# Kernel tuning notes

Hardware: AMD Instinct MI355X
Metric: run time of the kernel (lower is better)

Reference implementation:

```python
import jax, jax.numpy as jnp
import numpy as np

N = 100000        # nodes
E = 1600000       # edges
F_IN = 128        # input features
H = 64            # hidden
B = 256           # graphs in batch
MIN_SCORE = 1e-3  # SAGPooling min_score
TOL = 1e-7        # PyG topk tolerance
NEG = jnp.float32(-1e30)


def setup_inputs() -> dict:
    key = jax.random.key(0)
    ks = jax.random.split(key, 24)
    x = jax.random.normal(ks[0], (N, F_IN), jnp.float32)
    src = jax.random.randint(ks[1], (E,), 0, N, dtype=jnp.int32)
    dst = jax.random.randint(ks[2], (E,), 0, N, dtype=jnp.int32)
    batch = jnp.sort(jax.random.randint(ks[3], (N,), 0, B, dtype=jnp.int32))
    node_attention = jax.random.uniform(ks[4], (N,), jnp.float32)

    def lin(k, i, o):
        return jax.random.normal(k, (i, o), jnp.float32) / np.float32(np.sqrt(i))

    p = {
        'W11': lin(ks[5], F_IN, H), 'b11': jnp.zeros((H,), jnp.float32),
        'W12': lin(ks[6], H, H),    'b12': jnp.zeros((H,), jnp.float32),
        'gW1': lin(ks[7], H, 1),    'gb1': jnp.zeros((1,), jnp.float32),
        'W21': lin(ks[8], H, H),    'b21': jnp.zeros((H,), jnp.float32),
        'W22': lin(ks[9], H, H),    'b22': jnp.zeros((H,), jnp.float32),
        'gW2': lin(ks[10], H, 1),   'gb2': jnp.zeros((1,), jnp.float32),
        'W31': lin(ks[11], H, H),   'b31': jnp.zeros((H,), jnp.float32),
        'W32': lin(ks[12], H, H),   'b32': jnp.zeros((H,), jnp.float32),
        'Wl':  lin(ks[13], H, 1),   'bl': jnp.zeros((1,), jnp.float32),
    }
    return dict(x=x, src=src, dst=dst, batch=batch, node_attention=node_attention, **p)


def gin_conv(x, src, dst, emask, W1, b1, W2, b2):
    # GINConv, eps=0: mlp(x + sum_{j in N(i)} x_j), edges masked by emask
    agg = jax.ops.segment_sum(x[src] * emask[:, None], dst, num_segments=N)
    h = x + agg
    return jax.nn.relu(h @ W1 + b1) @ W2 + b2


def gcn_attn(x, src, dst, emask, nmask, W, b):
    # GCNConv(H,1) with self-loops + symmetric normalization on the masked graph
    h = x @ W  # [N,1]
    deg = jax.ops.segment_sum(emask, dst, num_segments=N) + nmask
    dinv = jnp.where(deg > 0, jax.lax.rsqrt(jnp.maximum(deg, 1e-12)), 0.0)
    coef = dinv[src] * dinv[dst] * emask
    out = jax.ops.segment_sum(h[src] * coef[:, None], dst, num_segments=N)
    out = out + h * (dinv * dinv * nmask)[:, None] + b
    return out[:, 0]


def seg_softmax(a, batch, nmask):
    am = jnp.where(nmask > 0, a, NEG)
    m = jax.ops.segment_max(am, batch, num_segments=B)
    e = jnp.where(nmask > 0, jnp.exp(a - m[batch]), 0.0)
    s = jax.ops.segment_sum(e, batch, num_segments=B)
    return e / jnp.maximum(s[batch], 1e-30)


def sag_pool(x, src, dst, emask, nmask, batch, W, b):
    attn = gcn_attn(x, src, dst, emask, nmask, W, b)
    score = seg_softmax(attn, batch, nmask)
    smax = jax.ops.segment_max(jnp.where(nmask > 0, score, NEG), batch, num_segments=B)
    thr = jnp.minimum(MIN_SCORE, smax[batch] - TOL)
    keep = ((nmask > 0) & (score > thr)).astype(x.dtype)
    x2 = x * (score * keep)[:, None]          # x[perm] * score[perm], masked form
    emask2 = emask * keep[src] * keep[dst]    # filter_adj
    return x2, emask2, keep, score


def reference(x, src, dst, batch, node_attention,
              W11, b11, W12, b12, gW1, gb1,
              W21, b21, W22, b22, gW2, gb2,
              W31, b31, W32, b32, Wl, bl):
    emask = jnp.ones((E,), x.dtype)
    nmask0 = jnp.ones((N,), x.dtype)

    h = jax.nn.relu(gin_conv(x, src, dst, emask, W11, b11, W12, b12))
    h, emask, keep1, _ = sag_pool(h, src, dst, emask, nmask0, batch, gW1, gb1)

    h = jax.nn.relu(gin_conv(h, src, dst, emask, W21, b21, W22, b22))
    h, emask, keep2, score2 = sag_pool(h, src, dst, emask, keep1, batch, gW2, gb2)

    ratio = jnp.sum(keep2) / jnp.float32(N)

    h = jax.nn.relu(gin_conv(h, src, dst, emask, W31, b31, W32, b32))

    # global max pool over surviving nodes
    hm = jnp.where(keep2[:, None] > 0, h, NEG)
    g = jax.ops.segment_max(hm, batch, num_segments=B)
    out = g @ Wl + bl  # [B,1]

    # attention KL loss; perm2 indexes the pool1-compacted array (as in the source)
    r1 = jnp.clip(jnp.cumsum(keep1).astype(jnp.int32) - 1, 0, N - 1)
    t = node_attention[r1]
    logp = jnp.log(score2 + 1e-14)
    kl = jnp.where(t > 0, t * jnp.log(jnp.maximum(t, 1e-38)), 0.0) - t * logp
    kl = kl * keep2
    s = jax.ops.segment_sum(kl, batch, num_segments=B)
    c = jax.ops.segment_sum(keep2, batch, num_segments=B)
    attn_loss = s / jnp.maximum(c, 1.0)  # scatter_mean

    return out, attn_loss, ratio
```

## Files before the change

### kernel.cpp

```cpp
#include <hip/hip_runtime.h>
#include <hip/hip_fp16.h>
#include <math.h>

#define NN 100000
#define NE 1600000
#define NB 256
#define NEGF (-1e30f)
#define NSCAN_BLK ((NN + 1023) / 1024)
#define GVB 1024
#define P_SORT 256
#define NBKT 391
#define HLEN (NBKT * P_SORT)
#define HSCAN_BLK ((HLEN + 1023) / 1024)
#define BKT_CAP 6144

__global__ void k_hist_coarse(const int* __restrict__ dst, const int* __restrict__ batch,
                              int* __restrict__ offs, int* __restrict__ H) {
    __shared__ int lh[NBKT];
    int p = blockIdx.x, tid = threadIdx.x;
    if (p == 0) {
        for (int g = tid; g <= NB; g += 256) {
            int lo = 0, hi = NN;
            while (lo < hi) { int mid = (lo + hi) >> 1; if (batch[mid] < g) lo = mid + 1; else hi = mid; }
            offs[g] = lo;
        }
    }
    for (int i = tid; i < NBKT; i += 256) lh[i] = 0;
    __syncthreads();
    int c0 = p * (NE / P_SORT), c1 = c0 + NE / P_SORT;
    for (int i = c0 + tid; i < c1; i += 256) atomicAdd(&lh[dst[i] >> 8], 1);
    __syncthreads();
    for (int i = tid; i < NBKT; i += 256) H[i * P_SORT + p] = lh[i];
}
__global__ void k_iscan_blk(const int* __restrict__ in, int* __restrict__ pref,
                            int* __restrict__ bsums, int len) {
    int blk = blockIdx.x, tid = threadIdx.x;
    int base = blk * 1024;
    int vals[4], tsum = 0;
    for (int j = 0; j < 4; ++j) {
        int idx = base + tid * 4 + j;
        int v = (idx < len) ? in[idx] : 0;
        vals[j] = tsum; tsum += v;
    }
    __shared__ int sh[256];
    sh[tid] = tsum; __syncthreads();
    for (int o = 1; o < 256; o <<= 1) {
        int v = (tid >= o) ? sh[tid - o] : 0;
        __syncthreads();
        sh[tid] += v;
        __syncthreads();
    }
    int excl = sh[tid] - tsum;
    for (int j = 0; j < 4; ++j) {
        int idx = base + tid * 4 + j;
        if (idx < len) pref[idx] = excl + vals[j];
    }
    if (tid == 255) bsums[blk] = sh[255];
}
__global__ void k_iscan_add(int* __restrict__ pref, const int* __restrict__ bsums, int len) {
    __shared__ int sh[256];
    int t = threadIdx.x;
    int sb = blockIdx.x >> 2;
    sh[t] = (t < sb) ? bsums[t] : 0;
    __syncthreads();
    for (int o = 128; o > 0; o >>= 1) { if (t < o) sh[t] += sh[t + o]; __syncthreads(); }
    int pre = sh[0];
    int idx = blockIdx.x * 256 + t;
    if (idx < len) pref[idx] += pre;
}
__global__ void k_scatter_pairs(const int* __restrict__ src, const int* __restrict__ dst,
                                const int* __restrict__ Hs, int2* __restrict__ ebuf) {
    __shared__ int curs[NBKT];
    int p = blockIdx.x, tid = threadIdx.x;
    for (int i = tid; i < NBKT; i += 256) curs[i] = Hs[i * P_SORT + p];
    __syncthreads();
    int c0 = p * (NE / P_SORT), c1 = c0 + NE / P_SORT;
    for (int i = c0 + tid; i < c1; i += 256) {
        int d = dst[i];
        int pos = atomicAdd(&curs[d >> 8], 1);
        ebuf[pos] = make_int2(src[i], d);
    }
}
__global__ void k_bucket_csr(const int2* __restrict__ ebuf, const int* __restrict__ Hs,
                             int* __restrict__ roffs, int* __restrict__ csrc) {
    __shared__ int hist2[256];
    __shared__ int curs2[256];
    __shared__ int sh[256];
    __shared__ int stage[BKT_CAP];
    int b = blockIdx.x, tid = threadIdx.x;
    int e0 = Hs[b * P_SORT];
    int e1 = (b + 1 < NBKT) ? Hs[(b + 1) * P_SORT] : NE;
    int n0 = b * 256;
    int cntb = e1 - e0;
    if (b == 0 && tid == 0) roffs[NN] = NE;
    hist2[tid] = 0;
    __syncthreads();
    for (int i = e0 + tid; i < e1; i += 256) atomicAdd(&hist2[ebuf[i].y & 255], 1);
    __syncthreads();
    int v = hist2[tid];
    sh[tid] = v; __syncthreads();
    for (int o = 1; o < 256; o <<= 1) {
        int u = (tid >= o) ? sh[tid - o] : 0;
        __syncthreads();
        sh[tid] += u;
        __syncthreads();
    }
    int excl = sh[tid] - v;
    int node = n0 + tid;
    if (node < NN) roffs[node] = e0 + excl;
    curs2[tid] = excl;
    __syncthreads();
    if (cntb <= BKT_CAP) {
        for (int i = e0 + tid; i < e1; i += 256) {
            int2 pr = ebuf[i];
            int pos = atomicAdd(&curs2[pr.y & 255], 1);
            stage[pos] = pr.x;
        }
        __syncthreads();
        for (int i = tid; i < cntb; i += 256) csrc[e0 + i] = stage[i];
    } else {
        for (int i = e0 + tid; i < e1; i += 256) {
            int2 pr = ebuf[i];
            int pos = atomicAdd(&curs2[pr.y & 255], 1);
            csrc[e0 + pos] = pr.x;
        }
    }
}

__global__ __launch_bounds__(256) void k_pre1_g(const float* __restrict__ x,
                                                const float* __restrict__ W,
                                                float* __restrict__ y) {
    __shared__ float lds[4][4 * 128];
    int tid = threadIdx.x, w = tid >> 6, l = tid & 63;
    float Wc[128];
#pragma unroll
    for (int k = 0; k < 128; ++k) Wc[k] = W[k * 64 + l];
    float* row = lds[w];
    int g = blockIdx.x * 4 + w;
    const int G = GVB * 4;
    for (int t = g; t < NN / 4; t += G) {
        int n0 = t * 4;
#pragma unroll
        for (int r = 0; r < 4; ++r) {
            row[r * 128 + l]      = x[(size_t)(n0 + r) * 128 + l];
            row[r * 128 + 64 + l] = x[(size_t)(n0 + r) * 128 + 64 + l];
        }
        __builtin_amdgcn_wave_barrier();
        float acc[4] = {0.f, 0.f, 0.f, 0.f};
#pragma unroll
        for (int k = 0; k < 128; k += 4) {
#pragma unroll
            for (int r = 0; r < 4; ++r) {
                float4 bv = *(const float4*)&row[r * 128 + k];
                acc[r] = fmaf(bv.x, Wc[k],     acc[r]);
                acc[r] = fmaf(bv.y, Wc[k + 1], acc[r]);
                acc[r] = fmaf(bv.z, Wc[k + 2], acc[r]);
                acc[r] = fmaf(bv.w, Wc[k + 3], acc[r]);
            }
        }
        __builtin_amdgcn_wave_barrier();
#pragma unroll
        for (int r = 0; r < 4; ++r) y[(size_t)(n0 + r) * 64 + l] = acc[r];
    }
}

__global__ __launch_bounds__(256) void k_pre23_h(const float* __restrict__ h,
                                                 const float* __restrict__ sk,
                                                 const float* __restrict__ W,
                                                 __half* __restrict__ yh) {
    __shared__ float lds[4][8 * 64];
    int tid = threadIdx.x, w = tid >> 6, l = tid & 63;
    float Wc[64];
#pragma unroll
    for (int k = 0; k < 64; ++k) Wc[k] = W[k * 64 + l];
    float* row = lds[w];
    int g = blockIdx.x * 4 + w;
    const int G = GVB * 4;
    for (int t = g; t < NN / 8; t += G) {
        int n0 = t * 8;
#pragma unroll
        for (int r = 0; r < 8; ++r) row[r * 64 + l] = h[(size_t)(n0 + r) * 64 + l];
        __builtin_amdgcn_wave_barrier();
        float acc[8] = {0.f, 0.f, 0.f, 0.f, 0.f, 0.f, 0.f, 0.f};
#pragma unroll
        for (int k = 0; k < 64; k += 4) {
#pragma unroll
            for (int r = 0; r < 8; ++r) {
                float4 bv = *(const float4*)&row[r * 64 + k];
                acc[r] = fmaf(bv.x, Wc[k],     acc[r]);
                acc[r] = fmaf(bv.y, Wc[k + 1], acc[r]);
                acc[r] = fmaf(bv.z, Wc[k + 2], acc[r]);
                acc[r] = fmaf(bv.w, Wc[k + 3], acc[r]);
            }
        }
        __builtin_amdgcn_wave_barrier();
#pragma unroll
        for (int r = 0; r < 8; ++r)
            yh[(size_t)(n0 + r) * 64 + l] = __float2half(acc[r] * sk[n0 + r]);
    }
}

__global__ __launch_bounds__(256) void k_post_g(const float* __restrict__ zp,
                                                const float* __restrict__ W2,
                                                const float* __restrict__ b2,
                                                const float* __restrict__ gW,
                                                const int* __restrict__ roffs,
                                                const int* __restrict__ cnt,
                                                const float* __restrict__ keep,
                                                float* __restrict__ hOut,
                                                float* __restrict__ hwd,
                                                float* __restrict__ dinv, int mode) {
    __shared__ float lds[4][8 * 64];
    int tid = threadIdx.x, w = tid >> 6, l = tid & 63;
    float Wc[64];
#pragma unroll
    for (int k = 0; k < 64; ++k) Wc[k] = W2[k * 64 + l];
    float b2v = b2[l];
    float gWv = (mode < 3) ? gW[l] : 0.f;
    float* row = lds[w];
    int g = blockIdx.x * 4 + w;
    const int G = GVB * 4;
    for (int t = g; t < NN / 8; t += G) {
        int n0 = t * 8;
#pragma unroll
        for (int r = 0; r < 8; ++r) row[r * 64 + l] = zp[(size_t)(n0 + r) * 64 + l];
        __builtin_amdgcn_wave_barrier();
        float acc[8];
#pragma unroll
        for (int r = 0; r < 8; ++r) acc[r] = b2v;
#pragma unroll
        for (int k = 0; k < 64; k += 4) {
#pragma unroll
            for (int r = 0; r < 8; ++r) {
                float4 bv = *(const float4*)&row[r * 64 + k];
                acc[r] = fmaf(bv.x, Wc[k],     acc[r]);
                acc[r] = fmaf(bv.y, Wc[k + 1], acc[r]);
                acc[r] = fmaf(bv.z, Wc[k + 2], acc[r]);
                acc[r] = fmaf(bv.w, Wc[k + 3], acc[r]);
            }
        }
        __builtin_amdgcn_wave_barrier();
#pragma unroll
        for (int r = 0; r < 8; ++r) {
            acc[r] = fmaxf(acc[r], 0.f);
            hOut[(size_t)(n0 + r) * 64 + l] = acc[r];
        }
        if (mode < 3) {
#pragma unroll
            for (int r = 0; r < 8; ++r) {
                float t2 = acc[r] * gWv;
                for (int o = 32; o > 0; o >>= 1) t2 += __shfl_down(t2, o, 64);
                if (l == 0) {
                    int n = n0 + r;
                    float di;
                    if (mode == 1) di = 1.f / sqrtf((float)(roffs[n + 1] - roffs[n]) + 1.f);
                    else di = (keep[n] != 0.f) ? 1.f / sqrtf((float)cnt[n] + 1.f) : 0.f;
                    dinv[n] = di;
                    hwd[n] = t2 * di;
                }
            }
        }
    }
}

__global__ void k_gather_y(const float* __restrict__ y, const int* __restrict__ roffs,
                           const int* __restrict__ csrc, const float* __restrict__ b1,
                           float* __restrict__ z) {
    int tid = threadIdx.x;
    int d = blockIdx.x * 16 + (tid >> 4);
    int l = tid & 15;
    const float4* y4 = (const float4*)y;
    float4 acc = y4[(size_t)d * 16 + l];
    int e0 = roffs[d], e1 = roffs[d + 1];
    int e = e0;
    for (; e + 3 < e1; e += 4) {
        int s0 = csrc[e], s1 = csrc[e + 1], s2 = csrc[e + 2], s3 = csrc[e + 3];
        float4 v0 = y4[(size_t)s0 * 16 + l];
        float4 v1 = y4[(size_t)s1 * 16 + l];
        float4 v2 = y4[(size_t)s2 * 16 + l];
        float4 v3 = y4[(size_t)s3 * 16 + l];
        acc.x += (v0.x + v1.x) + (v2.x + v3.x);
        acc.y += (v0.y + v1.y) + (v2.y + v3.y);
        acc.z += (v0.z + v1.z) + (v2.z + v3.z);
        acc.w += (v0.w + v1.w) + (v2.w + v3.w);
    }
    for (; e < e1; ++e) {
        float4 v0 = y4[(size_t)csrc[e] * 16 + l];
        acc.x += v0.x; acc.y += v0.y; acc.z += v0.z; acc.w += v0.w;
    }
    float4 o;
    o.x = fmaxf(acc.x + b1[4 * l],     0.f);
    o.y = fmaxf(acc.y + b1[4 * l + 1], 0.f);
    o.z = fmaxf(acc.z + b1[4 * l + 2], 0.f);
    o.w = fmaxf(acc.w + b1[4 * l + 3], 0.f);
    ((float4*)z)[(size_t)d * 16 + l] = o;
}

__global__ void k_gather_h(const __half* __restrict__ yh, const int* __restrict__ roffs,
                           const int* __restrict__ csrc, const float* __restrict__ keepd,
                           const float* __restrict__ sk, const float* __restrict__ b1,
                           float* __restrict__ z, int* __restrict__ cnt) {
    int tid = threadIdx.x;
    int d = blockIdx.x * 16 + (tid >> 4);
    int l = tid & 15;
    const float2* yv = (const float2*)yh;
    float2 raw = yv[(size_t)d * 16 + l];
    __half2 p0 = ((const __half2*)&raw)[0], p1 = ((const __half2*)&raw)[1];
    float4 acc = make_float4(__low2float(p0), __high2float(p0),
                             __low2float(p1), __high2float(p1));
    int c = 0;
    if (!keepd || keepd[d] != 0.f) {
        int e0 = roffs[d], e1 = roffs[d + 1];
        int e = e0;
        for (; e + 3 < e1; e += 4) {
            int s0 = csrc[e], s1 = csrc[e + 1], s2 = csrc[e + 2], s3 = csrc[e + 3];
            float2 r0 = yv[(size_t)s0 * 16 + l];
            float2 r1 = yv[(size_t)s1 * 16 + l];
            float2 r2 = yv[(size_t)s2 * 16 + l];
            float2 r3 = yv[(size_t)s3 * 16 + l];
#pragma unroll
            for (int j = 0; j < 4; ++j) {
                float2 rr = (j == 0) ? r0 : (j == 1) ? r1 : (j == 2) ? r2 : r3;
                __half2 a0 = ((const __half2*)&rr)[0], a1 = ((const __half2*)&rr)[1];
                acc.x += __low2float(a0); acc.y += __high2float(a0);
                acc.z += __low2float(a1); acc.w += __high2float(a1);
            }
            if (sk) c += (sk[s0] > 0.f) + (sk[s1] > 0.f) + (sk[s2] > 0.f) + (sk[s3] > 0.f);
        }
        for (; e < e1; ++e) {
            int s0 = csrc[e];
            float2 rr = yv[(size_t)s0 * 16 + l];
            __half2 a0 = ((const __half2*)&rr)[0], a1 = ((const __half2*)&rr)[1];
            acc.x += __low2float(a0); acc.y += __high2float(a0);
            acc.z += __low2float(a1); acc.w += __high2float(a1);
            if (sk) c += (sk[s0] > 0.f);
        }
    }
    float4 o;
    o.x = fmaxf(acc.x + b1[4 * l],     0.f);
    o.y = fmaxf(acc.y + b1[4 * l + 1], 0.f);
    o.z = fmaxf(acc.z + b1[4 * l + 2], 0.f);
    o.w = fmaxf(acc.w + b1[4 * l + 3], 0.f);
    ((float4*)z)[(size_t)d * 16 + l] = o;
    if (cnt && l == 0) cnt[d] = c;
}

__global__ void k_attn(const int* __restrict__ roffs, const int* __restrict__ csrc,
                       const float* __restrict__ hwd, const float* __restrict__ dinv,
                       const float* __restrict__ gb, float* __restrict__ attn) {
    int i = blockIdx.x * 256 + threadIdx.x;
    if (i >= NN) return;
    float sum = hwd[i];
    int e0 = roffs[i], e1 = roffs[i + 1];
    for (int e = e0; e < e1; ++e) sum += hwd[csrc[e]];
    attn[i] = dinv[i] * sum + gb[0];
}

__global__ void k_softmax_pool(const float* __restrict__ attn, const float* __restrict__ nmask,
                               const int* __restrict__ offs, float* __restrict__ score,
                               float* __restrict__ keep, float* __restrict__ sk) {
    int b = blockIdx.x, tid = threadIdx.x;
    int s0 = offs[b], s1 = offs[b + 1];
    __shared__ float red[256];
    float m = NEGF;
    for (int i = s0 + tid; i < s1; i += 256) {
        float nm = nmask ? nmask[i] : 1.f;
        if (nm > 0.f) m = fmaxf(m, attn[i]);
    }
    red[tid] = m; __syncthreads();
    for (int o = 128; o > 0; o >>= 1) { if (tid < o) red[tid] = fmaxf(red[tid], red[tid + o]); __syncthreads(); }
    m = red[0]; __syncthreads();
    float s = 0.f;
    for (int i = s0 + tid; i < s1; i += 256) {
        float nm = nmask ? nmask[i] : 1.f;
        if (nm > 0.f) s += expf(attn[i] - m);
    }
    red[tid] = s; __syncthreads();
    for (int o = 128; o > 0; o >>= 1) { if (tid < o) red[tid] += red[tid + o]; __syncthreads(); }
    s = red[0]; __syncthreads();
    float sden = fmaxf(s, 1e-30f);
    float smax = NEGF;
    for (int i = s0 + tid; i < s1; i += 256) {
        float nm = nmask ? nmask[i] : 1.f;
        float sc = (nm > 0.f) ? expf(attn[i] - m) / sden : 0.f;
        score[i] = sc;
        smax = fmaxf(smax, (nm > 0.f) ? sc : NEGF);
    }
    red[tid] = smax; __syncthreads();
    for (int o = 128; o > 0; o >>= 1) { if (tid < o) red[tid] = fmaxf(red[tid], red[tid + o]); __syncthreads(); }
    smax = red[0]; __syncthreads();
    float thr = fminf(1e-3f, smax - 1e-7f);
    for (int i = s0 + tid; i < s1; i += 256) {
        float nm = nmask ? nmask[i] : 1.f;
        float sc = score[i];
        float kp = (nm > 0.f && sc > thr) ? 1.f : 0.f;
        keep[i] = kp;
        sk[i] = sc * kp;
    }
}

__global__ void k_gmax_linear(const float* __restrict__ h, const float* __restrict__ keep2,
                              const int* __restrict__ offs, const float* __restrict__ Wl,
                              const float* __restrict__ bl, float* __restrict__ out) {
    int b = blockIdx.x, tid = threadIdx.x;
    int s0 = offs[b], s1 = offs[b + 1];
    int f = tid & 63, g = tid >> 6;
    float m = NEGF;
    for (int i = s0 + g; i < s1; i += 4)
        if (keep2[i] > 0.f) m = fmaxf(m, h[(size_t)i * 64 + f]);
    __shared__ float red[256];
    red[tid] = m; __syncthreads();
    if (g == 0) {
        m = fmaxf(fmaxf(red[f], red[64 + f]), fmaxf(red[128 + f], red[192 + f]));
        float v = m * Wl[f];
        for (int o = 32; o > 0; o >>= 1) v += __shfl_down(v, o, 64);
        if (f == 0) out[b] = v + bl[0];
    }
}

__global__ void k_scan1(const float* __restrict__ keep1, int* __restrict__ prefix,
                        int* __restrict__ bsums) {
    int blk = blockIdx.x, tid = threadIdx.x;
    int base = blk * 1024;
    int vals[4], tsum = 0;
    for (int j = 0; j < 4; ++j) {
        int idx = base + tid * 4 + j;
        int v = (idx < NN && keep1[idx] > 0.f) ? 1 : 0;
        tsum += v; vals[j] = tsum;
    }
    __shared__ int sh[256];
    sh[tid] = tsum; __syncthreads();
    for (int o = 1; o < 256; o <<= 1) {
        int v = (tid >= o) ? sh[tid - o] : 0;
        __syncthreads();
        sh[tid] += v;
        __syncthreads();
    }
    int excl = sh[tid] - tsum;
    for (int j = 0; j < 4; ++j) {
        int idx = base + tid * 4 + j;
        if (idx < NN) prefix[idx] = excl + vals[j];
    }
    if (tid == 255) bsums[blk] = sh[255];
}
__global__ void k_scan3(int* __restrict__ prefix, const int* __restrict__ bsums) {
    __shared__ int sh[256];
    int t = threadIdx.x;
    int sb = blockIdx.x >> 2;
    sh[t] = (t < sb) ? bsums[t] : 0;
    __syncthreads();
    for (int o = 128; o > 0; o >>= 1) { if (t < o) sh[t] += sh[t + o]; __syncthreads(); }
    int pre = sh[0];
    int idx = blockIdx.x * 256 + t;
    if (idx < NN) prefix[idx] += pre;
}

__global__ void k_kl(const float* __restrict__ score2, const float* __restrict__ keep2,
                     const int* __restrict__ prefix, const float* __restrict__ natt,
                     const int* __restrict__ offs, float* __restrict__ out_loss,
                     float* __restrict__ c_total) {
    int b = blockIdx.x, tid = threadIdx.x;
    int s0 = offs[b], s1 = offs[b + 1];
    float s = 0.f, c = 0.f;
    for (int i = s0 + tid; i < s1; i += 256) {
        if (keep2[i] > 0.f) {
            int r1 = prefix[i] - 1;
            r1 = max(0, min(r1, NN - 1));
            float t = natt[r1];
            float logp = logf(score2[i] + 1e-14f);
            float kl = ((t > 0.f) ? t * logf(fmaxf(t, 1e-38f)) : 0.f) - t * logp;
            s += kl; c += 1.f;
        }
    }
    __shared__ float rs[256], rc[256];
    rs[tid] = s; rc[tid] = c; __syncthreads();
    for (int o = 128; o > 0; o >>= 1) {
        if (tid < o) { rs[tid] += rs[tid + o]; rc[tid] += rc[tid + o]; }
        __syncthreads();
    }
    if (tid == 0) {
        out_loss[b] = rs[0] / fmaxf(rc[0], 1.f);
        atomicAdd(c_total, rc[0]);
    }
}
__global__ void k_final(const float* __restrict__ c_total, float* __restrict__ out) {
    out[0] = c_total[0] / (float)NN;
}

extern "C" void kernel_launch(void* const* d_in, const int* in_sizes, int n_in,
                              void* d_out, int out_size, void* d_ws, size_t ws_size,
                              hipStream_t stream) {
    const float* x    = (const float*)d_in[0];
    const int*   src  = (const int*)d_in[1];
    const int*   dst  = (const int*)d_in[2];
    const int*   batch= (const int*)d_in[3];
    const float* natt = (const float*)d_in[4];
    const float* W11 = (const float*)d_in[5],  *b11 = (const float*)d_in[6];
    const float* W12 = (const float*)d_in[7],  *b12 = (const float*)d_in[8];
    const float* gW1 = (const float*)d_in[9],  *gb1 = (const float*)d_in[10];
    const float* W21 = (const float*)d_in[11], *b21 = (const float*)d_in[12];
    const float* W22 = (const float*)d_in[13], *b22 = (const float*)d_in[14];
    const float* gW2 = (const float*)d_in[15], *gb2 = (const float*)d_in[16];
    const float* W31 = (const float*)d_in[17], *b31 = (const float*)d_in[18];
    const float* W32 = (const float*)d_in[19], *b32 = (const float*)d_in[20];
    const float* Wl  = (const float*)d_in[21], *bl  = (const float*)d_in[22];
    float* out = (float*)d_out;

    float* hA     = (float*)d_ws;
    float* hB     = hA + (size_t)NN * 64;
    float* ybuf   = hB + (size_t)NN * 64;
    float* zbuf   = ybuf + (size_t)NN * 64;
    float* hwd    = zbuf + (size_t)NN * 64;
    float* dinv   = hwd + NN;
    float* attn   = dinv + NN;
    float* score1 = attn + NN;
    float* keep1  = score1 + NN;
    float* sk1    = keep1 + NN;
    float* score2 = sk1 + NN;
    float* keep2  = score2 + NN;
    float* sk2    = keep2 + NN;
    int*   prefix = (int*)(sk2 + NN);
    int*   cnt    = prefix + NN;
    int*   roffs  = cnt + NN;
    int*   csrc   = roffs + NN + 1;
    int*   offs   = csrc + NE;
    int*   bsums  = offs + NB + 1;
    float* c_total= (float*)(bsums + 128);
    int*   H      = (int*)ybuf;
    int*   Hs     = H + HLEN;
    int2*  ebuf   = (int2*)zbuf;
    __half* yh    = (__half*)ybuf;

    const int nblk_n   = (NN + 255) / 256;
    const int nblk_n16 = NN / 16;

    k_hist_coarse<<<P_SORT, 256, 0, stream>>>(dst, batch, offs, H);
    k_iscan_blk<<<HSCAN_BLK, 256, 0, stream>>>(H, Hs, bsums, HLEN);
    k_iscan_add<<<(HLEN + 255) / 256, 256, 0, stream>>>(Hs, bsums, HLEN);
    k_scatter_pairs<<<P_SORT, 256, 0, stream>>>(src, dst, Hs, ebuf);
    k_bucket_csr<<<NBKT, 256, 0, stream>>>(ebuf, Hs, roffs, csrc);

    k_pre1_g<<<GVB, 256, 0, stream>>>(x, W11, ybuf);
    k_gather_y<<<nblk_n16, 256, 0, stream>>>(ybuf, roffs, csrc, b11, zbuf);
    k_post_g<<<GVB, 256, 0, stream>>>(zbuf, W12, b12, gW1, roffs, nullptr, nullptr,
                                      hA, hwd, dinv, 1);
    k_attn<<<nblk_n, 256, 0, stream>>>(roffs, csrc, hwd, dinv, gb1, attn);
    k_softmax_pool<<<NB, 256, 0, stream>>>(attn, nullptr, offs, score1, keep1, sk1);

    k_pre23_h<<<GVB, 256, 0, stream>>>(hA, sk1, W21, yh);
    k_gather_h<<<nblk_n16, 256, 0, stream>>>(yh, roffs, csrc, keep1, sk1, b21, zbuf, cnt);
    k_post_g<<<GVB, 256, 0, stream>>>(zbuf, W22, b22, gW2, roffs, cnt, keep1,
                                      hB, hwd, dinv, 2);
    k_attn<<<nblk_n, 256, 0, stream>>>(roffs, csrc, hwd, dinv, gb2, attn);
    k_softmax_pool<<<NB, 256, 0, stream>>>(attn, keep1, offs, score2, keep2, sk2);

    k_pre23_h<<<GVB, 256, 0, stream>>>(hB, sk2, W31, yh);
    k_gather_h<<<nblk_n16, 256, 0, stream>>>(yh, roffs, csrc, keep2, nullptr, b31, zbuf, nullptr);
    k_post_g<<<GVB, 256, 0, stream>>>(zbuf, W32, b32, nullptr, roffs, nullptr, nullptr,
                                      hA, nullptr, nullptr, 3);

    k_gmax_linear<<<NB, 256, 0, stream>>>(hA, keep2, offs, Wl, bl, out);

    k_scan1<<<NSCAN_BLK, 256, 0, stream>>>(keep1, prefix, bsums);
    k_scan3<<<nblk_n, 256, 0, stream>>>(prefix, bsums);
    hipMemsetAsync(c_total, 0, sizeof(float), stream);
    k_kl<<<NB, 256, 0, stream>>>(score2, keep2, prefix, natt, offs, out + NB, c_total);
    k_final<<<1, 1, 0, stream>>>(c_total, out + 2 * NB);
}
```

Baseline: 508.1 us.

## Fuse attention and softmax pooling per graph, bitmask keep flags, merge tail kernels

GCN attention and the segment softmax/top-k pooling now run in one per-graph kernel, with attention values held in shared memory, so the attn buffer round trip and one launch go away. Keep flags are packed into a 64-bit-per-word bitmask with ballot, and the masked gathers read that bitmask instead of float arrays, shrinking the random-access footprint. The global max-pool/linear and KL-loss kernels are merged into one kernel. In exchange, the attention step drops from one thread per node over the whole graph set to 256 per-graph blocks, and two small pack kernels are added.

```diff
diff --git a/kernel.cpp b/kernel.cpp
--- a/kernel.cpp
+++ b/kernel.cpp
@@ -13,6 +13,7 @@
 #define HLEN (NBKT * P_SORT)
 #define HSCAN_BLK ((HLEN + 1023) / 1024)
 #define BKT_CAP 6144
+#define NMASKW 1566
 
 __global__ void k_hist_coarse(const int* __restrict__ dst, const int* __restrict__ batch,
                               int* __restrict__ offs, int* __restrict__ H) {
@@ -297,8 +298,9 @@
 }
 
 __global__ void k_gather_h(const __half* __restrict__ yh, const int* __restrict__ roffs,
-                           const int* __restrict__ csrc, const float* __restrict__ keepd,
-                           const float* __restrict__ sk, const float* __restrict__ b1,
+                           const int* __restrict__ csrc,
+                           const unsigned long long* __restrict__ kmask,
+                           const float* __restrict__ b1,
                            float* __restrict__ z, int* __restrict__ cnt) {
     int tid = threadIdx.x;
     int d = blockIdx.x * 16 + (tid >> 4);
@@ -309,7 +311,7 @@
     float4 acc = make_float4(__low2float(p0), __high2float(p0),
                              __low2float(p1), __high2float(p1));
     int c = 0;
-    if (!keepd || keepd[d] != 0.f) {
+    if ((kmask[d >> 6] >> (d & 63)) & 1ull) {
         int e0 = roffs[d], e1 = roffs[d + 1];
         int e = e0;
         for (; e + 3 < e1; e += 4) {
@@ -325,7 +327,10 @@
                 acc.x += __low2float(a0); acc.y += __high2float(a0);
                 acc.z += __low2float(a1); acc.w += __high2float(a1);
             }
-            if (sk) c += (sk[s0] > 0.f) + (sk[s1] > 0.f) + (sk[s2] > 0.f) + (sk[s3] > 0.f);
+            if (cnt) c += (int)((kmask[s0 >> 6] >> (s0 & 63)) & 1ull)
+                        + (int)((kmask[s1 >> 6] >> (s1 & 63)) & 1ull)
+                        + (int)((kmask[s2 >> 6] >> (s2 & 63)) & 1ull)
+                        + (int)((kmask[s3 >> 6] >> (s3 & 63)) & 1ull);
         }
         for (; e < e1; ++e) {
             int s0 = csrc[e];
@@ -333,7 +338,7 @@
             __half2 a0 = ((const __half2*)&rr)[0], a1 = ((const __half2*)&rr)[1];
             acc.x += __low2float(a0); acc.y += __high2float(a0);
             acc.z += __low2float(a1); acc.w += __high2float(a1);
-            if (sk) c += (sk[s0] > 0.f);
+            if (cnt) c += (int)((kmask[s0 >> 6] >> (s0 & 63)) & 1ull);
         }
     }
     float4 o;
@@ -345,63 +350,76 @@
     if (cnt && l == 0) cnt[d] = c;
 }
 
-__global__ void k_attn(const int* __restrict__ roffs, const int* __restrict__ csrc,
+__global__ void k_pool(const int* __restrict__ roffs, const int* __restrict__ csrc,
                        const float* __restrict__ hwd, const float* __restrict__ dinv,
-                       const float* __restrict__ gb, float* __restrict__ attn) {
-    int i = blockIdx.x * 256 + threadIdx.x;
-    if (i >= NN) return;
-    float sum = hwd[i];
-    int e0 = roffs[i], e1 = roffs[i + 1];
-    for (int e = e0; e < e1; ++e) sum += hwd[csrc[e]];
-    attn[i] = dinv[i] * sum + gb[0];
-}
-
-__global__ void k_softmax_pool(const float* __restrict__ attn, const float* __restrict__ nmask,
-                               const int* __restrict__ offs, float* __restrict__ score,
-                               float* __restrict__ keep, float* __restrict__ sk) {
+                       const float* __restrict__ gb, const float* __restrict__ nmask,
+                       const int* __restrict__ offs, float* __restrict__ score,
+                       float* __restrict__ keep, float* __restrict__ sk) {
+    __shared__ float attn_s[2048];
+    __shared__ float red[256];
     int b = blockIdx.x, tid = threadIdx.x;
     int s0 = offs[b], s1 = offs[b + 1];
-    __shared__ float red[256];
+    int len = s1 - s0;
+    float gbv = gb[0];
+    for (int j = tid; j < len; j += 256) {
+        int i = s0 + j;
+        float a = NEGF;
+        if (!nmask || nmask[i] > 0.f) {
+            float sum = hwd[i];
+            int e0 = roffs[i], e1 = roffs[i + 1];
+            for (int e = e0; e < e1; ++e) sum += hwd[csrc[e]];
+            a = dinv[i] * sum + gbv;
+        }
+        attn_s[j] = a;
+    }
+    __syncthreads();
     float m = NEGF;
-    for (int i = s0 + tid; i < s1; i += 256) {
-        float nm = nmask ? nmask[i] : 1.f;
-        if (nm > 0.f) m = fmaxf(m, attn[i]);
-    }
+    for (int j = tid; j < len; j += 256) m = fmaxf(m, attn_s[j]);
     red[tid] = m; __syncthreads();
     for (int o = 128; o > 0; o >>= 1) { if (tid < o) red[tid] = fmaxf(red[tid], red[tid + o]); __syncthreads(); }
     m = red[0]; __syncthreads();
     float s = 0.f;
-    for (int i = s0 + tid; i < s1; i += 256) {
-        float nm = nmask ? nmask[i] : 1.f;
-        if (nm > 0.f) s += expf(attn[i] - m);
+    for (int j = tid; j < len; j += 256) {
+        float a = attn_s[j];
+        if (a > 0.5f * NEGF) s += expf(a - m);
     }
     red[tid] = s; __syncthreads();
     for (int o = 128; o > 0; o >>= 1) { if (tid < o) red[tid] += red[tid + o]; __syncthreads(); }
     s = red[0]; __syncthreads();
     float sden = fmaxf(s, 1e-30f);
     float smax = NEGF;
-    for (int i = s0 + tid; i < s1; i += 256) {
-        float nm = nmask ? nmask[i] : 1.f;
-        float sc = (nm > 0.f) ? expf(attn[i] - m) / sden : 0.f;
-        score[i] = sc;
-        smax = fmaxf(smax, (nm > 0.f) ? sc : NEGF);
+    for (int j = tid; j < len; j += 256) {
+        float a = attn_s[j];
+        float sc = (a > 0.5f * NEGF) ? expf(a - m) / sden : 0.f;
+        score[s0 + j] = sc;
+        attn_s[j] = sc;
+        smax = fmaxf(smax, (a > 0.5f * NEGF) ? sc : NEGF);
     }
     red[tid] = smax; __syncthreads();
     for (int o = 128; o > 0; o >>= 1) { if (tid < o) red[tid] = fmaxf(red[tid], red[tid + o]); __syncthreads(); }
     smax = red[0]; __syncthreads();
     float thr = fminf(1e-3f, smax - 1e-7f);
-    for (int i = s0 + tid; i < s1; i += 256) {
-        float nm = nmask ? nmask[i] : 1.f;
-        float sc = score[i];
-        float kp = (nm > 0.f && sc > thr) ? 1.f : 0.f;
-        keep[i] = kp;
-        sk[i] = sc * kp;
-    }
-}
-
-__global__ void k_gmax_linear(const float* __restrict__ h, const float* __restrict__ keep2,
-                              const int* __restrict__ offs, const float* __restrict__ Wl,
-                              const float* __restrict__ bl, float* __restrict__ out) {
+    for (int j = tid; j < len; j += 256) {
+        float sc = attn_s[j];
+        float kp = (sc > thr) ? 1.f : 0.f;
+        keep[s0 + j] = kp;
+        sk[s0 + j] = sc * kp;
+    }
+}
+
+__global__ void k_pack(const float* __restrict__ keep, unsigned long long* __restrict__ mask) {
+    int i = blockIdx.x * 256 + threadIdx.x;
+    float v = (i < NN) ? keep[i] : 0.f;
+    unsigned long long m = __ballot(v > 0.f);
+    if ((threadIdx.x & 63) == 0) mask[(unsigned)i >> 6] = m;
+}
+
+__global__ void k_tail(const float* __restrict__ h, const float* __restrict__ keep2,
+                       const int* __restrict__ offs, const float* __restrict__ Wl,
+                       const float* __restrict__ bl, const float* __restrict__ score2,
+                       const int* __restrict__ prefix, const float* __restrict__ natt,
+                       float* __restrict__ out, float* __restrict__ out_loss,
+                       float* __restrict__ c_total) {
     int b = blockIdx.x, tid = threadIdx.x;
     int s0 = offs[b], s1 = offs[b + 1];
     int f = tid & 63, g = tid >> 6;
@@ -416,6 +434,28 @@
         for (int o = 32; o > 0; o >>= 1) v += __shfl_down(v, o, 64);
         if (f == 0) out[b] = v + bl[0];
     }
+    __syncthreads();
+    float ssum = 0.f, c = 0.f;
+    for (int i = s0 + tid; i < s1; i += 256) {
+        if (keep2[i] > 0.f) {
+            int r1 = prefix[i] - 1;
+            r1 = max(0, min(r1, NN - 1));
+            float t = natt[r1];
+            float logp = logf(score2[i] + 1e-14f);
+            float kl = ((t > 0.f) ? t * logf(fmaxf(t, 1e-38f)) : 0.f) - t * logp;
+            ssum += kl; c += 1.f;
+        }
+    }
+    __shared__ float rs[256], rc[256];
+    rs[tid] = ssum; rc[tid] = c; __syncthreads();
+    for (int o = 128; o > 0; o >>= 1) {
+        if (tid < o) { rs[tid] += rs[tid + o]; rc[tid] += rc[tid + o]; }
+        __syncthreads();
+    }
+    if (tid == 0) {
+        out_loss[b] = rs[0] / fmaxf(rc[0], 1.f);
+        atomicAdd(c_total, rc[0]);
+    }
 }
 
 __global__ void k_scan1(const float* __restrict__ keep1, int* __restrict__ prefix,
@@ -455,34 +495,6 @@
     if (idx < NN) prefix[idx] += pre;
 }
 
-__global__ void k_kl(const float* __restrict__ score2, const float* __restrict__ keep2,
-                     const int* __restrict__ prefix, const float* __restrict__ natt,
-                     const int* __restrict__ offs, float* __restrict__ out_loss,
-                     float* __restrict__ c_total) {
-    int b = blockIdx.x, tid = threadIdx.x;
-    int s0 = offs[b], s1 = offs[b + 1];
-    float s = 0.f, c = 0.f;
-    for (int i = s0 + tid; i < s1; i += 256) {
-        if (keep2[i] > 0.f) {
-            int r1 = prefix[i] - 1;
-            r1 = max(0, min(r1, NN - 1));
-            float t = natt[r1];
-            float logp = logf(score2[i] + 1e-14f);
-            float kl = ((t > 0.f) ? t * logf(fmaxf(t, 1e-38f)) : 0.f) - t * logp;
-            s += kl; c += 1.f;
-        }
-    }
-    __shared__ float rs[256], rc[256];
-    rs[tid] = s; rc[tid] = c; __syncthreads();
-    for (int o = 128; o > 0; o >>= 1) {
-        if (tid < o) { rs[tid] += rs[tid + o]; rc[tid] += rc[tid + o]; }
-        __syncthreads();
-    }
-    if (tid == 0) {
-        out_loss[b] = rs[0] / fmaxf(rc[0], 1.f);
-        atomicAdd(c_total, rc[0]);
-    }
-}
 __global__ void k_final(const float* __restrict__ c_total, float* __restrict__ out) {
     out[0] = c_total[0] / (float)NN;
 }
@@ -512,8 +524,7 @@
     float* zbuf   = ybuf + (size_t)NN * 64;
     float* hwd    = zbuf + (size_t)NN * 64;
     float* dinv   = hwd + NN;
-    float* attn   = dinv + NN;
-    float* score1 = attn + NN;
+    float* score1 = dinv + NN;
     float* keep1  = score1 + NN;
     float* sk1    = keep1 + NN;
     float* score2 = sk1 + NN;
@@ -526,6 +537,8 @@
     int*   offs   = csrc + NE;
     int*   bsums  = offs + NB + 1;
     float* c_total= (float*)(bsums + 128);
+    unsigned long long* mask1 = (unsigned long long*)(((uintptr_t)(c_total + 1) + 7) & ~(uintptr_t)7);
+    unsigned long long* mask2 = mask1 + NMASKW;
     int*   H      = (int*)ybuf;
     int*   Hs     = H + HLEN;
     int2*  ebuf   = (int2*)zbuf;
@@ -544,26 +557,28 @@
     k_gather_y<<<nblk_n16, 256, 0, stream>>>(ybuf, roffs, csrc, b11, zbuf);
     k_post_g<<<GVB, 256, 0, stream>>>(zbuf, W12, b12, gW1, roffs, nullptr, nullptr,
                                       hA, hwd, dinv, 1);
-    k_attn<<<nblk_n, 256, 0, stream>>>(roffs, csrc, hwd, dinv, gb1, attn);
-    k_softmax_pool<<<NB, 256, 0, stream>>>(attn, nullptr, offs, score1, keep1, sk1);
+    k_pool<<<NB, 256, 0, stream>>>(roffs, csrc, hwd, dinv, gb1, nullptr, offs,
+                                   score1, keep1, sk1);
+    k_pack<<<nblk_n, 256, 0, stream>>>(keep1, mask1);
 
     k_pre23_h<<<GVB, 256, 0, stream>>>(hA, sk1, W21, yh);
-    k_gather_h<<<nblk_n16, 256, 0, stream>>>(yh, roffs, csrc, keep1, sk1, b21, zbuf, cnt);
+    k_gather_h<<<nblk_n16, 256, 0, stream>>>(yh, roffs, csrc, mask1, b21, zbuf, cnt);
     k_post_g<<<GVB, 256, 0, stream>>>(zbuf, W22, b22, gW2, roffs, cnt, keep1,
                                       hB, hwd, dinv, 2);
-    k_attn<<<nblk_n, 256, 0, stream>>>(roffs, csrc, hwd, dinv, gb2, attn);
-    k_softmax_pool<<<NB, 256, 0, stream>>>(attn, keep1, offs, score2, keep2, sk2);
+    k_pool<<<NB, 256, 0, stream>>>(roffs, csrc, hwd, dinv, gb2, keep1, offs,
+                                   score2, keep2, sk2);
+    k_pack<<<nblk_n, 256, 0, stream>>>(keep2, mask2);
 
     k_pre23_h<<<GVB, 256, 0, stream>>>(hB, sk2, W31, yh);
-    k_gather_h<<<nblk_n16, 256, 0, stream>>>(yh, roffs, csrc, keep2, nullptr, b31, zbuf, nullptr);
+    k_gather_h<<<nblk_n16, 256, 0, stream>>>(yh, roffs, csrc, mask2, b31, zbuf, nullptr);
     k_post_g<<<GVB, 256, 0, stream>>>(zbuf, W32, b32, nullptr, roffs, nullptr, nullptr,
                                       hA, nullptr, nullptr, 3);
 
-    k_gmax_linear<<<NB, 256, 0, stream>>>(hA, keep2, offs, Wl, bl, out);
-
     k_scan1<<<NSCAN_BLK, 256, 0, stream>>>(keep1, prefix, bsums);
     k_scan3<<<nblk_n, 256, 0, stream>>>(prefix, bsums);
+
     hipMemsetAsync(c_total, 0, sizeof(float), stream);
-    k_kl<<<NB, 256, 0, stream>>>(score2, keep2, prefix, natt, offs, out + NB, c_total);
+    k_tail<<<NB, 256, 0, stream>>>(hA, keep2, offs, Wl, bl, score2, prefix, natt,
+                                   out, out + NB, c_total);
     k_final<<<1, 1, 0, stream>>>(c_total, out + 2 * NB);
 }
```

Result: no change. 508.0 us (-0.0%).
